# Kernel optimization log

Measured on AMD Instinct MI355X. Metric: run time of the kernel, lower is better.

The kernel has to match this reference:

```python
import jax, jax.numpy as jnp
import numpy as np
from jax import lax

B, T, D, H = 64, 512, 512, 512


def setup_inputs() -> dict:
    key = jax.random.key(0)
    k1, k2 = jax.random.split(key)
    x = jax.random.normal(k1, (B, T, D), dtype=jnp.float32)
    # single fused gate weight: concat([h, x]) -> 4 gates of size H (f, i, o, c_bar)
    W = jax.random.normal(k2, (H + D, 4 * H), dtype=jnp.float32) * (1.0 / np.sqrt(H + D))
    b = jnp.zeros((4 * H,), dtype=jnp.float32)
    return {"x": x, "W": W, "b": b}


def reference(x, W, b):
    """LSTM per source math: c' = sig(f)*c + sig(i)*c_bar ; h' = sig(o)*c' (no tanh)."""
    Bb = x.shape[0]
    Hh = W.shape[1] // 4
    dt = x.dtype

    def step(carry, xt):
        h, c = carry
        z = jnp.concatenate([h, xt], axis=-1) @ W + b  # [B, 4H]
        f, i, o, c_bar = jnp.split(z, 4, axis=-1)
        c_new = jax.nn.sigmoid(f) * c + jax.nn.sigmoid(i) * c_bar
        h_new = jax.nn.sigmoid(o) * c_new
        return (h_new, c_new), h_new

    init = (jnp.zeros((Bb, Hh), dt), jnp.zeros((Bb, Hh), dt))
    _, hs = lax.scan(step, init, jnp.swapaxes(x, 0, 1))  # hs: [T, B, H]
    return jnp.swapaxes(hs, 0, 1)  # [B, T, H]
```

## Files before the change

### kernel.cpp

```cpp
#include <hip/hip_runtime.h>
#include <math.h>

#define Bz 64
#define Tz 512
#define Dz 512
#define Hz 512

#define WB_FLOATS   (64*1024*32)
#define HBUF_FLOATS (64*512)

__global__ __launch_bounds__(256) void zero_ws(float* __restrict__ p, int n) {
    int i = blockIdx.x * 256 + threadIdx.x;
    if (i < n) p[i] = 0.0f;
}

__global__ __launch_bounds__(256) void prep_w(const float* __restrict__ W,
                                              float* __restrict__ Wb) {
    int k = blockIdx.x;
    for (int it = 0; it < 8; ++it) {
        int col = it * 256 + threadIdx.x;
        float v = W[(size_t)k * 2048 + col];
        int g = col >> 9, rem = col & 511;
        int cg = rem >> 3, hc = rem & 7;
        int c = g * 8 + hc;
        Wb[((size_t)cg * 1024 + k) * 32 + c] = v;
    }
}

__global__ __launch_bounds__(256) void lstm_step(
    const float* __restrict__ x,
    const float* __restrict__ bias,
    const float* __restrict__ Wb,
    const float* __restrict__ hbr,
    float* __restrict__ hbw,
    float* __restrict__ cbuf,
    float* __restrict__ out,
    int t)
{
    const int cg  = blockIdx.x;
    const int sg  = blockIdx.y;
    const int tid = threadIdx.x;

    __shared__ float As[16 * 1028];
    __shared__ float zpart[8 * 512];
    __shared__ float zred[512];

    for (int it = 0; it < 16; ++it) {
        int fi = it * 256 + tid;
        int s  = fi >> 8;
        int k  = (fi & 255) * 4;
        const float* src;
        if (k < 512) src = hbr + (sg * 16 + s) * 512 + k;
        else         src = x + (size_t)(sg * 16 + s) * Tz * Dz
                             + (size_t)t * Dz + (k - 512);
        float4 v = *(const float4*)src;
        *(float4*)(As + s * 1028 + k) = v;
    }
    __syncthreads();

    const int ct = tid & 7;
    const int st = (tid >> 3) & 3;
    const int kw = tid >> 5;

    float acc[4][4];
#pragma unroll
    for (int i = 0; i < 4; ++i)
#pragma unroll
        for (int j = 0; j < 4; ++j) acc[i][j] = 0.0f;

    const float* wp = Wb + (size_t)cg * 1024 * 32 + (size_t)(kw * 128) * 32 + ct * 4;
    const float* ap = As + st * 4 * 1028 + kw * 128;

#pragma unroll 4
    for (int kk = 0; kk < 128; kk += 4) {
        float4 w0 = *(const float4*)(wp + (kk + 0) * 32);
        float4 w1 = *(const float4*)(wp + (kk + 1) * 32);
        float4 w2 = *(const float4*)(wp + (kk + 2) * 32);
        float4 w3 = *(const float4*)(wp + (kk + 3) * 32);
        float4 a0 = *(const float4*)(ap + 0 * 1028 + kk);
        float4 a1 = *(const float4*)(ap + 1 * 1028 + kk);
        float4 a2 = *(const float4*)(ap + 2 * 1028 + kk);
        float4 a3 = *(const float4*)(ap + 3 * 1028 + kk);
#define FMA_ROW(i, ai)                                              \
        acc[i][0] += ai.x * w0.x + ai.y * w1.x + ai.z * w2.x + ai.w * w3.x; \
        acc[i][1] += ai.x * w0.y + ai.y * w1.y + ai.z * w2.y + ai.w * w3.y; \
        acc[i][2] += ai.x * w0.z + ai.y * w1.z + ai.z * w2.z + ai.w * w3.z; \
        acc[i][3] += ai.x * w0.w + ai.y * w1.w + ai.z * w2.w + ai.w * w3.w;
        FMA_ROW(0, a0)
        FMA_ROW(1, a1)
        FMA_ROW(2, a2)
        FMA_ROW(3, a3)
#undef FMA_ROW
    }

#pragma unroll
    for (int i = 0; i < 4; ++i) {
        float4 v = make_float4(acc[i][0], acc[i][1], acc[i][2], acc[i][3]);
        *(float4*)(zpart + kw * 512 + (st * 4 + i) * 32 + ct * 4) = v;
    }
    __syncthreads();

    {
        int o = tid * 2;
        float z0 = 0.0f, z1 = 0.0f;
#pragma unroll
        for (int w = 0; w < 8; ++w) {
            float2 v = *(const float2*)(zpart + w * 512 + o);
            z0 += v.x; z1 += v.y;
        }
        *(float2*)(zred + o) = make_float2(z0, z1);
    }
    __syncthreads();

    if (tid < 128) {
        int s  = tid >> 3;
        int hc = tid & 7;
        int colb = cg * 8 + hc;
        float zf = zred[s * 32 + hc]       + bias[colb];
        float zi = zred[s * 32 + 8 + hc]   + bias[512 + colb];
        float zo = zred[s * 32 + 16 + hc]  + bias[1024 + colb];
        float zc = zred[s * 32 + 24 + hc]  + bias[1536 + colb];

        int cidx = (sg * 64 + cg) * 128 + tid;
        float cold = cbuf[cidx];
        float sf = 1.0f / (1.0f + expf(-zf));
        float si = 1.0f / (1.0f + expf(-zi));
        float so = 1.0f / (1.0f + expf(-zo));
        float cnew = sf * cold + si * zc;
        float h = so * cnew;
        cbuf[cidx] = cnew;

        hbw[(sg * 16 + s) * 512 + colb] = h;
        out[(size_t)(sg * 16 + s) * Tz * Hz + (size_t)t * Hz + colb] = h;
    }
}

extern "C" void kernel_launch(void* const* d_in, const int* in_sizes, int n_in,
                              void* d_out, int out_size, void* d_ws, size_t ws_size,
                              hipStream_t stream) {
    const float* x    = (const float*)d_in[0];
    const float* W    = (const float*)d_in[1];
    const float* bias = (const float*)d_in[2];
    float* out = (float*)d_out;

    char* ws = (char*)d_ws;
    float* Wb   = (float*)ws;
    float* hbuf = (float*)(ws + (size_t)WB_FLOATS * 4);
    float* cbuf = hbuf + 2 * HBUF_FLOATS;

    zero_ws<<<384, 256, 0, stream>>>(hbuf, 98304);
    prep_w<<<1024, 256, 0, stream>>>(W, Wb);

    for (int t = 0; t < Tz; ++t) {
        float* hr = hbuf + (t & 1) * HBUF_FLOATS;
        float* hw = hbuf + ((t + 1) & 1) * HBUF_FLOATS;
        lstm_step<<<dim3(64, 4), 256, 0, stream>>>(x, bias, Wb, hr, hw, cbuf, out, t);
    }
}
```

Before: 7.560 ms.

## Precompute input projection with GEMM and run recurrence in persistent cooperative kernel

Hoists the x@W_x input projection plus bias out of the time loop into one large tiled GEMM over all timesteps. The recurrence then runs as a single persistent cooperative kernel of 256 blocks. Each block keeps its 8 weight columns resident in LDS and holds its cell state in registers, and blocks synchronise each step through an atomic arrival counter instead of 512 separate kernel launches. This removes per-step launch overhead and repeated weight reloads. In exchange it needs a large workspace, at least 256 CUs and cooperative launch support, and a spin-barrier that breaks out after a bounded iteration count, which could silently corrupt results if the barrier times out.

```diff
diff --git a/kernel.cpp b/kernel.cpp
--- a/kernel.cpp
+++ b/kernel.cpp
@@ -1,10 +1,211 @@
 #include <hip/hip_runtime.h>
 #include <math.h>
+#include <stdint.h>
 
 #define Bz 64
 #define Tz 512
 #define Dz 512
 #define Hz 512
+
+__device__ __forceinline__ int col_of_n(int n) {
+    int cc = n & 7;
+    int cg = n >> 3;
+    return (cc >> 1) * 512 + cg * 2 + (cc & 1);
+}
+
+#define ZX_FLOATS  ((size_t)32768 * 2048)
+#define GHB_FLOATS (2 * 64 * 512)
+#define ARR_INTS   512
+#define NEW_WS_BYTES (ZX_FLOATS * 4 + (size_t)GHB_FLOATS * 4 + (size_t)ARR_INTS * 4)
+
+#define HS_STRIDE 516
+#define WT_OFF    33024
+#define ZSC_OFF   37152
+#define ZRED_OFF  39232
+#define LDS_FLOATS 39752
+#define LDS_BYTES (LDS_FLOATS * 4)
+
+__global__ __launch_bounds__(256) void zero_init(int* __restrict__ p, int n) {
+    int i = blockIdx.x * 256 + threadIdx.x;
+    if (i < n) p[i] = 0;
+}
+
+__global__ __launch_bounds__(256) void zx_gemm(const float* __restrict__ x,
+                                               const float* __restrict__ W,
+                                               const float* __restrict__ bias,
+                                               float* __restrict__ Zx) {
+    __shared__ float As[16][132];
+    __shared__ float Bs[16][132];
+    const int mb = blockIdx.x;
+    const int nb = blockIdx.y;
+    const int tid = threadIdx.x;
+    const int tx = tid & 15, ty = tid >> 4;
+
+    float acc[8][8];
+#pragma unroll
+    for (int i = 0; i < 8; ++i)
+#pragma unroll
+        for (int j = 0; j < 8; ++j) acc[i][j] = 0.f;
+
+    const int n_local = tid & 127;
+    const int kp = tid >> 7;
+    const int cB = col_of_n(nb * 128 + n_local);
+
+    for (int k0 = 0; k0 < 512; k0 += 16) {
+#pragma unroll
+        for (int it = 0; it < 2; ++it) {
+            int fi = it * 256 + tid;
+            int r = fi >> 2, k4 = (fi & 3) * 4;
+            int t = mb * 2 + (r >> 6), s = r & 63;
+            float4 v = *(const float4*)(x + (size_t)s * (Tz * Dz) + (size_t)t * Dz + k0 + k4);
+            As[k4 + 0][r] = v.x;
+            As[k4 + 1][r] = v.y;
+            As[k4 + 2][r] = v.z;
+            As[k4 + 3][r] = v.w;
+        }
+        {
+            const float* wp = W + (size_t)(512 + k0 + kp * 8) * 2048 + cB;
+#pragma unroll
+            for (int ii = 0; ii < 8; ++ii)
+                Bs[kp * 8 + ii][n_local] = wp[(size_t)ii * 2048];
+        }
+        __syncthreads();
+#pragma unroll
+        for (int k = 0; k < 16; ++k) {
+            float a[8], b[8];
+            *(float4*)(a)     = *(const float4*)&As[k][ty * 8];
+            *(float4*)(a + 4) = *(const float4*)&As[k][ty * 8 + 4];
+            *(float4*)(b)     = *(const float4*)&Bs[k][tx * 8];
+            *(float4*)(b + 4) = *(const float4*)&Bs[k][tx * 8 + 4];
+#pragma unroll
+            for (int i = 0; i < 8; ++i)
+#pragma unroll
+                for (int j = 0; j < 8; ++j) acc[i][j] = fmaf(a[i], b[j], acc[i][j]);
+        }
+        __syncthreads();
+    }
+#pragma unroll
+    for (int i = 0; i < 8; ++i) {
+        size_t m = (size_t)mb * 128 + ty * 8 + i;
+        float* zp = Zx + m * 2048 + nb * 128 + tx * 8;
+        float4 v0, v1;
+        int nbase = nb * 128 + tx * 8;
+        v0.x = acc[i][0] + bias[col_of_n(nbase + 0)];
+        v0.y = acc[i][1] + bias[col_of_n(nbase + 1)];
+        v0.z = acc[i][2] + bias[col_of_n(nbase + 2)];
+        v0.w = acc[i][3] + bias[col_of_n(nbase + 3)];
+        v1.x = acc[i][4] + bias[col_of_n(nbase + 4)];
+        v1.y = acc[i][5] + bias[col_of_n(nbase + 5)];
+        v1.z = acc[i][6] + bias[col_of_n(nbase + 6)];
+        v1.w = acc[i][7] + bias[col_of_n(nbase + 7)];
+        *(float4*)(zp) = v0;
+        *(float4*)(zp + 4) = v1;
+    }
+}
+
+__device__ __forceinline__ void gload_lds16(const float* g, float* l) {
+    __builtin_amdgcn_global_load_lds((const __attribute__((address_space(1))) void*)g,
+                                     (__attribute__((address_space(3))) void*)l,
+                                     16, 0, 0);
+}
+
+__global__ void __launch_bounds__(512) lstm_persist(const float* __restrict__ W,
+                                                    const float* __restrict__ Zx,
+                                                    float* __restrict__ ghb,
+                                                    int* __restrict__ arrive,
+                                                    float* __restrict__ out) {
+    extern __shared__ float lds[];
+    float* hs   = lds;
+    float* wt   = lds + WT_OFF;
+    float* zsc  = lds + ZSC_OFF;
+    float* zred = lds + ZRED_OFF;
+
+    const int bx  = blockIdx.x;
+    const int tid = threadIdx.x;
+    const int lane = tid & 63;
+    const int wid  = tid >> 6;
+
+    for (int i = tid; i < 8 * 512; i += 512) {
+        int cc = i >> 9, k = i & 511;
+        wt[cc * HS_STRIDE + k] = W[(size_t)k * 2048 + col_of_n(bx * 8 + cc)];
+    }
+    float c_reg = 0.0f;
+    __syncthreads();
+
+    const int cp = tid & 3;
+    const int sp = (tid >> 2) & 31;
+    const int kq = tid >> 7;
+
+    const float* ap0 = hs + sp * HS_STRIDE + kq * 128;
+    const float* ap1 = hs + (sp + 32) * HS_STRIDE + kq * 128;
+    const float* wp0 = wt + (cp * 2) * HS_STRIDE + kq * 128;
+    const float* wp1 = wt + (cp * 2 + 1) * HS_STRIDE + kq * 128;
+
+    for (int t = 0; t < Tz; ++t) {
+        const float* hsrc = ghb + (size_t)(t & 1) * (64 * 512);
+#pragma unroll
+        for (int r8 = 0; r8 < 8; ++r8) {
+            int row = wid * 8 + r8;
+#pragma unroll
+            for (int half = 0; half < 2; ++half) {
+                gload_lds16(hsrc + row * 512 + half * 256 + lane * 4,
+                            hs + row * HS_STRIDE + half * 256);
+            }
+        }
+        float zx_reg = Zx[((size_t)t * 64 + (tid >> 3)) * 2048 + bx * 8 + (tid & 7)];
+        __syncthreads();
+
+        float a00 = 0.f, a01 = 0.f, a10 = 0.f, a11 = 0.f;
+#pragma unroll 4
+        for (int kk = 0; kk < 128; kk += 4) {
+            float4 av0 = *(const float4*)(ap0 + kk);
+            float4 av1 = *(const float4*)(ap1 + kk);
+            float4 wv0 = *(const float4*)(wp0 + kk);
+            float4 wv1 = *(const float4*)(wp1 + kk);
+            a00 += av0.x * wv0.x + av0.y * wv0.y + av0.z * wv0.z + av0.w * wv0.w;
+            a01 += av0.x * wv1.x + av0.y * wv1.y + av0.z * wv1.z + av0.w * wv1.w;
+            a10 += av1.x * wv0.x + av1.y * wv0.y + av1.z * wv0.z + av1.w * wv0.w;
+            a11 += av1.x * wv1.x + av1.y * wv1.y + av1.z * wv1.z + av1.w * wv1.w;
+        }
+        *(float2*)(zsc + kq * 520 + sp * 8 + cp * 2)        = make_float2(a00, a01);
+        *(float2*)(zsc + kq * 520 + (sp + 32) * 8 + cp * 2) = make_float2(a10, a11);
+        __syncthreads();
+
+        zred[tid] = zsc[tid] + zsc[520 + tid] + zsc[2 * 520 + tid] + zsc[3 * 520 + tid] + zx_reg;
+        __syncthreads();
+
+        if (tid < 128) {
+            int s = tid >> 1, j = tid & 1;
+            float zf = zred[s * 8 + 0 + j];
+            float zi = zred[s * 8 + 2 + j];
+            float zo = zred[s * 8 + 4 + j];
+            float zc = zred[s * 8 + 6 + j];
+            float sf = 1.f / (1.f + expf(-zf));
+            float si = 1.f / (1.f + expf(-zi));
+            float so = 1.f / (1.f + expf(-zo));
+            float cnew = sf * c_reg + si * zc;
+            c_reg = cnew;
+            float h = so * cnew;
+            int hc = bx * 2 + j;
+            ghb[(size_t)((t + 1) & 1) * (64 * 512) + s * 512 + hc] = h;
+            out[(size_t)s * (Tz * Hz) + (size_t)t * Hz + hc] = h;
+        }
+        __syncthreads();
+
+        if (tid == 0) {
+            __threadfence();
+            atomicAdd(&arrive[t], 1);
+            int iters = 0;
+            while (__hip_atomic_load(&arrive[t], __ATOMIC_RELAXED,
+                                     __HIP_MEMORY_SCOPE_AGENT) < 256) {
+                __builtin_amdgcn_s_sleep(2);
+                if (++iters >= 100000) break;
+            }
+            __threadfence();
+        }
+        __syncthreads();
+    }
+}
 
 #define WB_FLOATS   (64*1024*32)
 #define HBUF_FLOATS (64*512)
@@ -28,14 +229,10 @@
 }
 
 __global__ __launch_bounds__(256) void lstm_step(
-    const float* __restrict__ x,
-    const float* __restrict__ bias,
-    const float* __restrict__ Wb,
-    const float* __restrict__ hbr,
-    float* __restrict__ hbw,
-    float* __restrict__ cbuf,
-    float* __restrict__ out,
-    int t)
+    const float* __restrict__ x, const float* __restrict__ bias,
+    const float* __restrict__ Wb, const float* __restrict__ hbr,
+    float* __restrict__ hbw, float* __restrict__ cbuf,
+    float* __restrict__ out, int t)
 {
     const int cg  = blockIdx.x;
     const int sg  = blockIdx.y;
@@ -51,8 +248,7 @@
         int k  = (fi & 255) * 4;
         const float* src;
         if (k < 512) src = hbr + (sg * 16 + s) * 512 + k;
-        else         src = x + (size_t)(sg * 16 + s) * Tz * Dz
-                             + (size_t)t * Dz + (k - 512);
+        else         src = x + (size_t)(sg * 16 + s) * Tz * Dz + (size_t)t * Dz + (k - 512);
         float4 v = *(const float4*)src;
         *(float4*)(As + s * 1028 + k) = v;
     }
@@ -135,6 +331,23 @@
     }
 }
 
+static void run_legacy(const float* x, const float* W, const float* bias,
+                       float* out, void* d_ws, hipStream_t stream) {
+    char* ws = (char*)d_ws;
+    float* Wb   = (float*)ws;
+    float* hbuf = (float*)(ws + (size_t)WB_FLOATS * 4);
+    float* cbuf = hbuf + 2 * HBUF_FLOATS;
+
+    zero_ws<<<384, 256, 0, stream>>>(hbuf, 98304);
+    prep_w<<<1024, 256, 0, stream>>>(W, Wb);
+
+    for (int t = 0; t < Tz; ++t) {
+        float* hr = hbuf + (t & 1) * HBUF_FLOATS;
+        float* hw = hbuf + ((t + 1) & 1) * HBUF_FLOATS;
+        lstm_step<<<dim3(64, 4), 256, 0, stream>>>(x, bias, Wb, hr, hw, cbuf, out, t);
+    }
+}
+
 extern "C" void kernel_launch(void* const* d_in, const int* in_sizes, int n_in,
                               void* d_out, int out_size, void* d_ws, size_t ws_size,
                               hipStream_t stream) {
@@ -143,17 +356,49 @@
     const float* bias = (const float*)d_in[2];
     float* out = (float*)d_out;
 
-    char* ws = (char*)d_ws;
-    float* Wb   = (float*)ws;
-    float* hbuf = (float*)(ws + (size_t)WB_FLOATS * 4);
-    float* cbuf = hbuf + 2 * HBUF_FLOATS;
-
-    zero_ws<<<384, 256, 0, stream>>>(hbuf, 98304);
-    prep_w<<<1024, 256, 0, stream>>>(W, Wb);
-
-    for (int t = 0; t < Tz; ++t) {
-        float* hr = hbuf + (t & 1) * HBUF_FLOATS;
-        float* hw = hbuf + ((t + 1) & 1) * HBUF_FLOATS;
-        lstm_step<<<dim3(64, 4), 256, 0, stream>>>(x, bias, Wb, hr, hw, cbuf, out, t);
-    }
-}
+    static int mode = -1;
+    if (mode < 0) {
+        int ok = (ws_size >= NEW_WS_BYTES);
+        if (ok) {
+            int dev = 0;
+            if (hipGetDevice(&dev) != hipSuccess) ok = 0;
+            int coop = 0, ncu = 0;
+            if (ok) {
+                hipDeviceGetAttribute(&coop, hipDeviceAttributeCooperativeLaunch, dev);
+                hipDeviceGetAttribute(&ncu, hipDeviceAttributeMultiprocessorCount, dev);
+                if (!coop || ncu < 256) ok = 0;
+            }
+            if (ok && hipFuncSetAttribute((const void*)lstm_persist,
+                        hipFuncAttributeMaxDynamicSharedMemorySize,
+                        (int)LDS_BYTES) != hipSuccess) ok = 0;
+            if (ok) {
+                int nblk = 0;
+                if (hipOccupancyMaxActiveBlocksPerMultiprocessor(&nblk,
+                        lstm_persist, 512, LDS_BYTES) != hipSuccess || nblk < 1)
+                    ok = 0;
+            }
+        }
+        mode = ok ? 1 : 0;
+    }
+
+    if (mode == 1) {
+        float* Zx   = (float*)d_ws;
+        float* ghb  = Zx + ZX_FLOATS;
+        int* arrive = (int*)(ghb + GHB_FLOATS);
+
+        zero_init<<<dim3((GHB_FLOATS + ARR_INTS + 255) / 256), 256, 0, stream>>>(
+            (int*)ghb, GHB_FLOATS + ARR_INTS);
+        zx_gemm<<<dim3(256, 16), 256, 0, stream>>>(x, W, bias, Zx);
+
+        const float* Wp = W; const float* Zxp = Zx;
+        float* ghbp = ghb; int* arrp = arrive; float* outp = out;
+        void* args[] = {(void*)&Wp, (void*)&Zxp, (void*)&ghbp, (void*)&arrp, (void*)&outp};
+        hipError_t e = hipLaunchCooperativeKernel((const void*)lstm_persist,
+                                                  dim3(256), dim3(512),
+                                                  args, (unsigned)LDS_BYTES, stream);
+        if (e == hipSuccess) return;
+        mode = 0;
+    }
+
+    run_legacy(x, W, bias, out, d_ws, stream);
+}
```

Result: slower. 7.825 ms (+3.5%).

## Replace per-timestep launches with a persistent fused LSTM kernel and grid barrier

Applied to the files above, without the earlier changes.

Swaps 512 per-timestep kernel launches for one persistent kernel of 256 blocks. Each block holds its slice of W (8 gate columns) in LDS, keeps the cell state in registers, and computes the x-projection before waiting on an atomic arrival counter for the previous step's h. This removes launch overhead and repeated weight reloads from global memory, and overlaps the x GEMM with the barrier wait. It relies on all 256 blocks being co-resident, and the spin-wait gives up after a bounded number of iterations, which could produce wrong results under contention.

```diff
diff --git a/kernel.cpp b/kernel.cpp
--- a/kernel.cpp
+++ b/kernel.cpp
@@ -1,10 +1,177 @@
 #include <hip/hip_runtime.h>
 #include <math.h>
+#include <stdint.h>
 
 #define Bz 64
 #define Tz 512
 #define Dz 512
 #define Hz 512
+
+__device__ __forceinline__ int wcol_of(int bx, int cc) {
+    return (cc >> 1) * 512 + bx * 2 + (cc & 1);
+}
+
+#define GHB_FLOATS (2 * 64 * 512)
+#define ARR_INTS   513
+#define FUSED_WS_BYTES ((size_t)GHB_FLOATS * 4 + (size_t)ARR_INTS * 4)
+
+#define A_STRIDE  516
+#define W_STRIDE  1044
+#define WT_OFF    16512
+#define ZSC_OFF   24864
+#define ZRED_OFF  33184
+#define POOL_FL   33696
+
+__global__ __launch_bounds__(256) void zero_init(int* __restrict__ p, int n) {
+    int i = blockIdx.x * 256 + threadIdx.x;
+    if (i < n) p[i] = 0;
+}
+
+__device__ __forceinline__ void gload_lds16(const float* g, float* l) {
+    __builtin_amdgcn_global_load_lds((const __attribute__((address_space(1))) void*)g,
+                                     (__attribute__((address_space(3))) void*)l,
+                                     16, 0, 0);
+}
+
+__device__ __forceinline__ void stage32(const float* __restrict__ src_base,
+                                        size_t row_stride, float* __restrict__ A,
+                                        int wid, int lane) {
+#pragma unroll
+    for (int rr = 0; rr < 4; ++rr) {
+        int r = wid * 4 + rr;
+#pragma unroll
+        for (int half = 0; half < 2; ++half)
+            gload_lds16(src_base + (size_t)r * row_stride + half * 256 + lane * 4,
+                        A + r * A_STRIDE + half * 256);
+    }
+}
+
+__device__ __forceinline__ void gemm_half(const float* __restrict__ A,
+                                          const float* __restrict__ wt,
+                                          int ksrc, int kq, int sh, int c2,
+                                          float acc[4][2]) {
+    const int kb = kq * 32;
+    const float* w0p = wt + (2 * c2)     * W_STRIDE + ksrc + kb;
+    const float* w1p = wt + (2 * c2 + 1) * W_STRIDE + ksrc + kb;
+#pragma unroll
+    for (int kk = 0; kk < 32; kk += 4) {
+        float4 w0 = *(const float4*)(w0p + kk);
+        float4 w1 = *(const float4*)(w1p + kk);
+#pragma unroll
+        for (int i = 0; i < 4; ++i) {
+            float4 a = *(const float4*)(A + (sh + 8 * i) * A_STRIDE + kb + kk);
+            acc[i][0] += a.x * w0.x + a.y * w0.y + a.z * w0.z + a.w * w0.w;
+            acc[i][1] += a.x * w1.x + a.y * w1.y + a.z * w1.z + a.w * w1.w;
+        }
+    }
+}
+
+__global__ void __launch_bounds__(512) lstm_fused(const float* __restrict__ x,
+                                                  const float* __restrict__ W,
+                                                  const float* __restrict__ bias,
+                                                  float* __restrict__ ghb,
+                                                  int* __restrict__ arrive,
+                                                  float* __restrict__ out) {
+    __shared__ float pool[POOL_FL];
+    float* A    = pool;
+    float* wt   = pool + WT_OFF;
+    float* zsc  = pool + ZSC_OFF;
+    float* zred = pool + ZRED_OFF;
+
+    const int bx   = blockIdx.x;
+    const int tid  = threadIdx.x;
+    const int lane = tid & 63;
+    const int wid  = tid >> 6;
+
+    for (int i = tid; i < 8 * 1024; i += 512) {
+        int cc = i >> 10, k = i & 1023;
+        wt[cc * W_STRIDE + k] = W[(size_t)k * 2048 + wcol_of(bx, cc)];
+    }
+    float c_reg = 0.0f;
+    __syncthreads();
+
+    const int c2 = tid & 3;
+    const int sh = (tid >> 2) & 7;
+    const int kq = tid >> 5;
+
+    for (int t = 0; t < Tz; ++t) {
+        float accA[4][2] = {{0.f,0.f},{0.f,0.f},{0.f,0.f},{0.f,0.f}};
+        float accB[4][2] = {{0.f,0.f},{0.f,0.f},{0.f,0.f},{0.f,0.f}};
+
+        const float* xt = x + (size_t)t * Dz;
+        stage32(xt, (size_t)Tz * Dz, A, wid, lane);
+        __syncthreads();
+        gemm_half(A, wt, 512, kq, sh, c2, accA);
+        __syncthreads();
+        stage32(xt + (size_t)32 * Tz * Dz, (size_t)Tz * Dz, A, wid, lane);
+        __syncthreads();
+        gemm_half(A, wt, 512, kq, sh, c2, accB);
+        __syncthreads();
+
+        if (t > 0) {
+            if (tid == 0) {
+                int iters = 0;
+                while (__hip_atomic_load(&arrive[t], __ATOMIC_RELAXED,
+                                         __HIP_MEMORY_SCOPE_AGENT) < 256) {
+                    __builtin_amdgcn_s_sleep(1);
+                    if (++iters >= 100000) break;
+                }
+                __threadfence();
+            }
+            __syncthreads();
+        }
+
+        const float* hsrc = ghb + (size_t)(t & 1) * (64 * 512);
+        stage32(hsrc, 512, A, wid, lane);
+        __syncthreads();
+        gemm_half(A, wt, 0, kq, sh, c2, accA);
+        __syncthreads();
+        stage32(hsrc + 32 * 512, 512, A, wid, lane);
+        __syncthreads();
+        gemm_half(A, wt, 0, kq, sh, c2, accB);
+
+#pragma unroll
+        for (int i = 0; i < 4; ++i) {
+            *(float2*)(zsc + kq * 520 + (sh + 8 * i) * 8 + 2 * c2) =
+                make_float2(accA[i][0], accA[i][1]);
+            *(float2*)(zsc + kq * 520 + (32 + sh + 8 * i) * 8 + 2 * c2) =
+                make_float2(accB[i][0], accB[i][1]);
+        }
+        __syncthreads();
+
+        {
+            float zs = 0.f;
+#pragma unroll
+            for (int q = 0; q < 16; ++q) zs += zsc[q * 520 + tid];
+            int cc = tid & 7;
+            zred[tid] = zs + bias[wcol_of(bx, cc)];
+        }
+        __syncthreads();
+
+        if (tid < 128) {
+            int s = tid >> 1, j = tid & 1;
+            float zf = zred[s * 8 + 0 + j];
+            float zi = zred[s * 8 + 2 + j];
+            float zo = zred[s * 8 + 4 + j];
+            float zc = zred[s * 8 + 6 + j];
+            float sf = 1.f / (1.f + expf(-zf));
+            float si = 1.f / (1.f + expf(-zi));
+            float so = 1.f / (1.f + expf(-zo));
+            float cnew = sf * c_reg + si * zc;
+            c_reg = cnew;
+            float h = so * cnew;
+            int hc = bx * 2 + j;
+            ghb[(size_t)((t + 1) & 1) * (64 * 512) + s * 512 + hc] = h;
+            out[(size_t)s * (Tz * Hz) + (size_t)t * Hz + hc] = h;
+        }
+        __syncthreads();
+
+        if (tid == 0 && t + 1 < Tz) {
+            __threadfence();
+            atomicAdd(&arrive[t + 1], 1);
+        }
+    }
+}
 
 #define WB_FLOATS   (64*1024*32)
 #define HBUF_FLOATS (64*512)
@@ -28,14 +195,10 @@
 }
 
 __global__ __launch_bounds__(256) void lstm_step(
-    const float* __restrict__ x,
-    const float* __restrict__ bias,
-    const float* __restrict__ Wb,
-    const float* __restrict__ hbr,
-    float* __restrict__ hbw,
-    float* __restrict__ cbuf,
-    float* __restrict__ out,
-    int t)
+    const float* __restrict__ x, const float* __restrict__ bias,
+    const float* __restrict__ Wb, const float* __restrict__ hbr,
+    float* __restrict__ hbw, float* __restrict__ cbuf,
+    float* __restrict__ out, int t)
 {
     const int cg  = blockIdx.x;
     const int sg  = blockIdx.y;
@@ -51,8 +214,7 @@
         int k  = (fi & 255) * 4;
         const float* src;
         if (k < 512) src = hbr + (sg * 16 + s) * 512 + k;
-        else         src = x + (size_t)(sg * 16 + s) * Tz * Dz
-                             + (size_t)t * Dz + (k - 512);
+        else         src = x + (size_t)(sg * 16 + s) * Tz * Dz + (size_t)t * Dz + (k - 512);
         float4 v = *(const float4*)src;
         *(float4*)(As + s * 1028 + k) = v;
     }
@@ -135,6 +297,23 @@
     }
 }
 
+static void run_legacy(const float* x, const float* W, const float* bias,
+                       float* out, void* d_ws, hipStream_t stream) {
+    char* ws = (char*)d_ws;
+    float* Wb   = (float*)ws;
+    float* hbuf = (float*)(ws + (size_t)WB_FLOATS * 4);
+    float* cbuf = hbuf + 2 * HBUF_FLOATS;
+
+    zero_ws<<<384, 256, 0, stream>>>(hbuf, 98304);
+    prep_w<<<1024, 256, 0, stream>>>(W, Wb);
+
+    for (int t = 0; t < Tz; ++t) {
+        float* hr = hbuf + (t & 1) * HBUF_FLOATS;
+        float* hw = hbuf + ((t + 1) & 1) * HBUF_FLOATS;
+        lstm_step<<<dim3(64, 4), 256, 0, stream>>>(x, bias, Wb, hr, hw, cbuf, out, t);
+    }
+}
+
 extern "C" void kernel_launch(void* const* d_in, const int* in_sizes, int n_in,
                               void* d_out, int out_size, void* d_ws, size_t ws_size,
                               hipStream_t stream) {
@@ -143,17 +322,15 @@
     const float* bias = (const float*)d_in[2];
     float* out = (float*)d_out;
 
-    char* ws = (char*)d_ws;
-    float* Wb   = (float*)ws;
-    float* hbuf = (float*)(ws + (size_t)WB_FLOATS * 4);
-    float* cbuf = hbuf + 2 * HBUF_FLOATS;
-
-    zero_ws<<<384, 256, 0, stream>>>(hbuf, 98304);
-    prep_w<<<1024, 256, 0, stream>>>(W, Wb);
-
-    for (int t = 0; t < Tz; ++t) {
-        float* hr = hbuf + (t & 1) * HBUF_FLOATS;
-        float* hw = hbuf + ((t + 1) & 1) * HBUF_FLOATS;
-        lstm_step<<<dim3(64, 4), 256, 0, stream>>>(x, bias, Wb, hr, hw, cbuf, out, t);
-    }
-}
+    if (ws_size < FUSED_WS_BYTES) {
+        run_legacy(x, W, bias, out, d_ws, stream);
+        return;
+    }
+
+    float* ghb  = (float*)d_ws;
+    int* arrive = (int*)(ghb + GHB_FLOATS);
+
+    zero_init<<<dim3((GHB_FLOATS + ARR_INTS + 255) / 256), 256, 0, stream>>>(
+        (int*)ghb, GHB_FLOATS + ARR_INTS);
+    lstm_fused<<<dim3(256), dim3(512), 0, stream>>>(x, W, bias, ghb, arrive, out);
+}
```

Measured after the change: 26.13 ms. 3.46x slower.

## Replace per-timestep launches with a persistent fused LSTM kernel and grid barrier

Applied to the files above, without the earlier changes.

Replaces 512 separate per-step kernel launches with one persistent kernel of 256 blocks, each keeping its slice of W in registers (8 columns × 8 k per thread). Timesteps are synchronized across blocks through atomic arrival counters in global memory, and h is read back from the output tensor. Inputs are staged into LDS with asynchronous global_load_lds in a double-buffered quarter pipeline, partial sums are reduced with wave shuffles, and the cell state stays in registers. This removes launch overhead and repeated weight reads, but relies on all 256 blocks being co-resident, and the spin wait has a timeout that could break correctness.

```diff
diff --git a/kernel.cpp b/kernel.cpp
--- a/kernel.cpp
+++ b/kernel.cpp
@@ -1,10 +1,193 @@
 #include <hip/hip_runtime.h>
 #include <math.h>
+#include <stdint.h>
 
 #define Bz 64
 #define Tz 512
 #define Dz 512
 #define Hz 512
+
+__device__ __forceinline__ int wcol_of(int bx, int cc) {
+    return (cc >> 1) * 512 + bx * 2 + (cc & 1);
+}
+
+#define ARR_INTS 516
+#define ZBUF_FL  512
+#define FUSED_WS_BYTES ((size_t)(ARR_INTS + ZBUF_FL) * 4)
+
+#define A_ST    1028
+#define A_FL    (16 * A_ST)
+#define ZSC_ST  132
+#define POOL_FL (2 * A_FL + 8 * ZSC_ST)
+
+__global__ __launch_bounds__(256) void zero_init(int* __restrict__ p, int n) {
+    int i = blockIdx.x * 256 + threadIdx.x;
+    if (i < n) p[i] = 0;
+}
+
+__device__ __forceinline__ void gload_lds16(const float* g, float* l) {
+    __builtin_amdgcn_global_load_lds((const __attribute__((address_space(1))) void*)g,
+                                     (__attribute__((address_space(3))) void*)l,
+                                     16, 0, 0);
+}
+
+__device__ __forceinline__ void stage_q(float* __restrict__ Ab,
+                                        const float* __restrict__ x,
+                                        const float* __restrict__ out,
+                                        const float* __restrict__ zbuf,
+                                        int t, int q, int wid, int lane) {
+#pragma unroll
+    for (int rr = 0; rr < 2; ++rr) {
+        int r = wid * 2 + rr;
+        int s = q * 16 + r;
+        const float* xs = x + (size_t)s * (Tz * Dz) + (size_t)t * Dz;
+        const float* hs = (t == 0) ? zbuf
+                        : out + (size_t)s * (Tz * Hz) + (size_t)(t - 1) * Hz;
+        float* arow = Ab + r * A_ST;
+        gload_lds16(hs + lane * 4,       arow);
+        gload_lds16(hs + 256 + lane * 4, arow + 256);
+        gload_lds16(xs + lane * 4,       arow + 512);
+        gload_lds16(xs + 256 + lane * 4, arow + 768);
+    }
+}
+
+template <int QQ, bool LAST>
+__device__ __forceinline__ void quarter_body(const float* __restrict__ Ab,
+                                             float* __restrict__ zsc,
+                                             int tid, int lane, int wid, int rg, int koff,
+                                             const float (&wreg)[8][8],
+                                             const float (&bias_r)[4],
+                                             float& c_reg, float& h_reg) {
+    if (LAST) { asm volatile("s_waitcnt vmcnt(0)" ::: "memory"); }
+    else      { asm volatile("s_waitcnt vmcnt(8)" ::: "memory"); }
+    __builtin_amdgcn_s_barrier();
+    __builtin_amdgcn_sched_barrier(0);
+
+    float acc[4][8];
+#pragma unroll
+    for (int rr = 0; rr < 4; ++rr) {
+        const float* ar = Ab + (rg * 4 + rr) * A_ST + koff;
+        float4 a0 = *(const float4*)(ar);
+        float4 a1 = *(const float4*)(ar + 4);
+#pragma unroll
+        for (int c = 0; c < 8; ++c) {
+            acc[rr][c] = a0.x * wreg[0][c] + a0.y * wreg[1][c]
+                       + a0.z * wreg[2][c] + a0.w * wreg[3][c]
+                       + a1.x * wreg[4][c] + a1.y * wreg[5][c]
+                       + a1.z * wreg[6][c] + a1.w * wreg[7][c];
+        }
+    }
+
+#pragma unroll
+    for (int m = 1; m < 16; m <<= 1)
+#pragma unroll
+        for (int rr = 0; rr < 4; ++rr)
+#pragma unroll
+            for (int c = 0; c < 8; ++c)
+                acc[rr][c] += __shfl_xor(acc[rr][c], m, 64);
+
+    if ((lane & 15) == 0) {
+#pragma unroll
+        for (int rr = 0; rr < 4; ++rr) {
+            int cell = (rg * 4 + rr) * 8;
+            *(float4*)(zsc + wid * ZSC_ST + cell) =
+                make_float4(acc[rr][0], acc[rr][1], acc[rr][2], acc[rr][3]);
+            *(float4*)(zsc + wid * ZSC_ST + cell + 4) =
+                make_float4(acc[rr][4], acc[rr][5], acc[rr][6], acc[rr][7]);
+        }
+    }
+    asm volatile("s_waitcnt lgkmcnt(0)" ::: "memory");
+    __builtin_amdgcn_s_barrier();
+    __builtin_amdgcn_sched_barrier(0);
+
+    if (tid < 128 && (tid >> 5) == QQ) {
+        int lr = (tid >> 1) & 15, j = tid & 1;
+        float zg[4];
+#pragma unroll
+        for (int g = 0; g < 4; ++g) {
+            float zz = bias_r[g];
+#pragma unroll
+            for (int kw = 0; kw < 8; ++kw)
+                zz += zsc[kw * ZSC_ST + lr * 8 + g * 2 + j];
+            zg[g] = zz;
+        }
+        float sf = 1.f / (1.f + expf(-zg[0]));
+        float si = 1.f / (1.f + expf(-zg[1]));
+        float so = 1.f / (1.f + expf(-zg[2]));
+        c_reg = sf * c_reg + si * zg[3];
+        h_reg = so * c_reg;
+    }
+}
+
+__global__ void __launch_bounds__(512) lstm_fused2(
+        const float* __restrict__ x, const float* __restrict__ W,
+        const float* __restrict__ bias, int* __restrict__ arrive,
+        const float* __restrict__ zbuf, float* __restrict__ out) {
+    __shared__ float pool[POOL_FL];
+    float* A0  = pool;
+    float* A1  = pool + A_FL;
+    float* zsc = pool + 2 * A_FL;
+
+    const int bx   = blockIdx.x;
+    const int tid  = threadIdx.x;
+    const int lane = tid & 63;
+    const int wid  = tid >> 6;
+    const int rg   = lane >> 4;
+    const int kq   = wid * 16 + (lane & 15);
+    const int koff = kq * 8;
+
+    float wreg[8][8];
+#pragma unroll
+    for (int kk = 0; kk < 8; ++kk)
+#pragma unroll
+        for (int c = 0; c < 8; ++c)
+            wreg[kk][c] = W[(size_t)(koff + kk) * 2048 + wcol_of(bx, c)];
+
+    float bias_r[4] = {0.f, 0.f, 0.f, 0.f};
+    if (tid < 128) {
+        int j = tid & 1;
+#pragma unroll
+        for (int g = 0; g < 4; ++g) bias_r[g] = bias[wcol_of(bx, g * 2 + j)];
+    }
+    const int s_own = tid >> 1, j_own = tid & 1;
+    float c_reg = 0.f, h_reg = 0.f;
+
+    for (int t = 0; t < Tz; ++t) {
+        if (t > 0) {
+            if (tid == 0) {
+                int it = 0;
+                while (__hip_atomic_load(arrive + (t - 1), __ATOMIC_RELAXED,
+                                         __HIP_MEMORY_SCOPE_AGENT) < 256) {
+                    __builtin_amdgcn_s_sleep(2);
+                    if (++it > 20000) break;
+                }
+            }
+            __builtin_amdgcn_s_barrier();
+            __builtin_amdgcn_sched_barrier(0);
+        }
+
+        stage_q(A0, x, out, zbuf, t, 0, wid, lane);
+        stage_q(A1, x, out, zbuf, t, 1, wid, lane);
+        quarter_body<0, false>(A0, zsc, tid, lane, wid, rg, koff, wreg, bias_r, c_reg, h_reg);
+        stage_q(A0, x, out, zbuf, t, 2, wid, lane);
+        quarter_body<1, false>(A1, zsc, tid, lane, wid, rg, koff, wreg, bias_r, c_reg, h_reg);
+        stage_q(A1, x, out, zbuf, t, 3, wid, lane);
+        quarter_body<2, false>(A0, zsc, tid, lane, wid, rg, koff, wreg, bias_r, c_reg, h_reg);
+        quarter_body<3, true >(A1, zsc, tid, lane, wid, rg, koff, wreg, bias_r, c_reg, h_reg);
+
+        if (tid < 128) {
+            __hip_atomic_store(out + (size_t)s_own * (Tz * Hz) + (size_t)t * Hz
+                                   + bx * 2 + j_own,
+                               h_reg, __ATOMIC_RELAXED, __HIP_MEMORY_SCOPE_AGENT);
+        }
+        asm volatile("s_waitcnt vmcnt(0)" ::: "memory");
+        __builtin_amdgcn_s_barrier();
+        __builtin_amdgcn_sched_barrier(0);
+        if (tid == 0)
+            __hip_atomic_fetch_add(arrive + t, 1, __ATOMIC_RELAXED,
+                                   __HIP_MEMORY_SCOPE_AGENT);
+    }
+}
 
 #define WB_FLOATS   (64*1024*32)
 #define HBUF_FLOATS (64*512)
@@ -28,14 +211,10 @@
 }
 
 __global__ __launch_bounds__(256) void lstm_step(
-    const float* __restrict__ x,
-    const float* __restrict__ bias,
-    const float* __restrict__ Wb,
-    const float* __restrict__ hbr,
-    float* __restrict__ hbw,
-    float* __restrict__ cbuf,
-    float* __restrict__ out,
-    int t)
+    const float* __restrict__ x, const float* __restrict__ bias,
+    const float* __restrict__ Wb, const float* __restrict__ hbr,
+    float* __restrict__ hbw, float* __restrict__ cbuf,
+    float* __restrict__ out, int t)
 {
     const int cg  = blockIdx.x;
     const int sg  = blockIdx.y;
@@ -51,8 +230,7 @@
         int k  = (fi & 255) * 4;
         const float* src;
         if (k < 512) src = hbr + (sg * 16 + s) * 512 + k;
-        else         src = x + (size_t)(sg * 16 + s) * Tz * Dz
-                             + (size_t)t * Dz + (k - 512);
+        else         src = x + (size_t)(sg * 16 + s) * Tz * Dz + (size_t)t * Dz + (k - 512);
         float4 v = *(const float4*)src;
         *(float4*)(As + s * 1028 + k) = v;
     }
@@ -135,6 +313,23 @@
     }
 }
 
+static void run_legacy(const float* x, const float* W, const float* bias,
+                       float* out, void* d_ws, hipStream_t stream) {
+    char* ws = (char*)d_ws;
+    float* Wb   = (float*)ws;
+    float* hbuf = (float*)(ws + (size_t)WB_FLOATS * 4);
+    float* cbuf = hbuf + 2 * HBUF_FLOATS;
+
+    zero_ws<<<384, 256, 0, stream>>>(hbuf, 98304);
+    prep_w<<<1024, 256, 0, stream>>>(W, Wb);
+
+    for (int t = 0; t < Tz; ++t) {
+        float* hr = hbuf + (t & 1) * HBUF_FLOATS;
+        float* hw = hbuf + ((t + 1) & 1) * HBUF_FLOATS;
+        lstm_step<<<dim3(64, 4), 256, 0, stream>>>(x, bias, Wb, hr, hw, cbuf, out, t);
+    }
+}
+
 extern "C" void kernel_launch(void* const* d_in, const int* in_sizes, int n_in,
                               void* d_out, int out_size, void* d_ws, size_t ws_size,
                               hipStream_t stream) {
@@ -143,17 +338,15 @@
     const float* bias = (const float*)d_in[2];
     float* out = (float*)d_out;
 
-    char* ws = (char*)d_ws;
-    float* Wb   = (float*)ws;
-    float* hbuf = (float*)(ws + (size_t)WB_FLOATS * 4);
-    float* cbuf = hbuf + 2 * HBUF_FLOATS;
-
-    zero_ws<<<384, 256, 0, stream>>>(hbuf, 98304);
-    prep_w<<<1024, 256, 0, stream>>>(W, Wb);
-
-    for (int t = 0; t < Tz; ++t) {
-        float* hr = hbuf + (t & 1) * HBUF_FLOATS;
-        float* hw = hbuf + ((t + 1) & 1) * HBUF_FLOATS;
-        lstm_step<<<dim3(64, 4), 256, 0, stream>>>(x, bias, Wb, hr, hw, cbuf, out, t);
-    }
-}
+    if (ws_size < FUSED_WS_BYTES) {
+        run_legacy(x, W, bias, out, d_ws, stream);
+        return;
+    }
+
+    int* arrive = (int*)d_ws;
+    float* zbuf = (float*)((char*)d_ws + ARR_INTS * 4);
+
+    zero_init<<<dim3((ARR_INTS + ZBUF_FL + 255) / 256), 256, 0, stream>>>(
+        (int*)d_ws, ARR_INTS + ZBUF_FL);
+    lstm_fused2<<<dim3(256), dim3(512), 0, stream>>>(x, W, bias, arrive, zbuf, out);
+}
```

After: 12.60 ms. 1.67x slower.
